# Kernel tuning notes

Measured on AMD Instinct MI355X. Metric: run time of the kernel, lower is better.

The kernel has to match this reference:

```python
import jax, jax.numpy as jnp
import numpy as np

B = 2
SEQ = 384            # args.seq_len (per-stock sub-sequence length)
N_AUX = 4            # len(args.aux_tickers)
S = SEQ * N_AUX + 1  # global separator token + tiled sub-sequences
D_MODEL = 512
NHEAD = 8
HEAD_DIM = 64
ROPE = 32            # qk_rope_dim
KV_C = 256
Q_C = 384
D_FF = 1536
H2 = NHEAD * 2       # differential attention sub-heads
DH = HEAD_DIM // 2
RH = ROPE // 2
EPS = 1.1920929e-07  # torch RMSNorm default eps (fp32 machine eps)
SCALING = 1.0 / ((HEAD_DIM + ROPE) // 2)
LAMBDA_INIT = 0.8 - 0.6 * float(np.exp(-0.3 * 0))  # depth=0 -> 0.2


def rmsnorm(x, w, eps=EPS):
    return x * jax.lax.rsqrt(jnp.mean(jnp.square(x), -1, keepdims=True) + eps) * w


def apply_rope(xs, cos, sin):
    # xs: [B, N_AUX, SEQ, H2, RH]; cos/sin: [SEQ, RH//2]
    xr = xs[..., 0::2]
    xi = xs[..., 1::2]
    c = cos[None, None, :, None, :]
    s = sin[None, None, :, None, :]
    yr = xr * c - xi * s
    yi = xr * s + xi * c
    return jnp.stack([yr, yi], axis=-1).reshape(xs.shape)


def _build_mask():
    causal = np.triu(np.ones((SEQ, SEQ), np.bool_), 1)
    tiled = np.tile(causal, (N_AUX, N_AUX))
    m = np.ones((S, S), np.bool_)
    m[:, 0] = False          # everyone attends to global separator
    m[1:, 1:] = tiled
    return jnp.asarray(m)[None, None]  # [1,1,S,S], True = masked


MASK = _build_mask()


def setup_inputs() -> dict:
    key = jax.random.key(0)
    ks = jax.random.split(key, 16)

    def w(k, shape, std=0.02):
        return jax.random.normal(k, shape, jnp.float32) * std

    x = jax.random.normal(ks[0], (B, S, D_MODEL), jnp.float32)
    # rope table: complex [SEQ, ROPE//4] stored as (cos, sin)
    pairs = ROPE // 4
    inv = 1.0 / (10000.0 ** (np.arange(pairs, dtype=np.float64) / pairs))
    ang = np.outer(np.arange(SEQ), inv)
    freqs = jnp.asarray(np.stack([np.cos(ang), np.sin(ang)], -1), jnp.float32)
    return {
        'x': x,
        'freqs': freqs,
        'W_kv_down': w(ks[1], (D_MODEL, KV_C + ROPE)),
        'W_q_down': w(ks[2], (D_MODEL, Q_C)),
        'W_kv_up': w(ks[3], (KV_C, NHEAD * HEAD_DIM * 2)),
        'W_q_up': w(ks[4], (Q_C, NHEAD * (HEAD_DIM + ROPE))),
        'kv_norm_w': jnp.ones((KV_C,), jnp.float32),
        'q_norm_w': jnp.ones((Q_C,), jnp.float32),
        'W_o': w(ks[5], (NHEAD * HEAD_DIM, D_MODEL)),
        'lambda_q1': w(ks[6], (DH,), 0.1),
        'lambda_k1': w(ks[7], (DH,), 0.1),
        'lambda_q2': w(ks[8], (DH,), 0.1),
        'lambda_k2': w(ks[9], (DH,), 0.1),
        'head_norm_w': jnp.ones((HEAD_DIM,), jnp.float32),
        'norm1_w': jnp.ones((D_MODEL,), jnp.float32),
        'norm2_w': jnp.ones((D_MODEL,), jnp.float32),
        'W_ff_in': w(ks[10], (D_MODEL, 2 * D_FF)),
        'W_ff_out': w(ks[11], (D_FF, D_MODEL)),
    }


def reference(x, freqs, W_kv_down, W_q_down, W_kv_up, W_q_up, kv_norm_w, q_norm_w,
              W_o, lambda_q1, lambda_k1, lambda_q2, lambda_k2, head_norm_w,
              norm1_w, norm2_w, W_ff_in, W_ff_out):
    cos, sin = freqs[..., 0], freqs[..., 1]
    # ---- attention block (pre-norm) ----
    h = rmsnorm(x, norm1_w)
    ckv_full = h @ W_kv_down                               # [B,S,KV_C+ROPE]
    c_kv, k_rope = ckv_full[..., :KV_C], ckv_full[..., KV_C:]
    kv = (rmsnorm(c_kv, kv_norm_w) @ W_kv_up).reshape(B, S, NHEAD, 2 * HEAD_DIM)
    k, v = kv[..., :HEAD_DIM], kv[..., HEAD_DIM:]
    k = k.reshape(B, S, H2, DH)
    qf = (rmsnorm(h @ W_q_down, q_norm_w) @ W_q_up).reshape(B, S, NHEAD, HEAD_DIM + ROPE)
    q, q_rope = qf[..., :HEAD_DIM], qf[..., HEAD_DIM:]
    q = q.reshape(B, S, H2, DH)
    k_rope = jnp.broadcast_to(k_rope[:, :, None, :], (B, S, NHEAD, ROPE)).reshape(B, S, H2, RH)
    q_rope = q_rope.reshape(B, S, H2, RH)
    # split off global separator token, rope per sub-sequence
    q_sep, q_rot = q_rope[:, :1], q_rope[:, 1:].reshape(B, N_AUX, SEQ, H2, RH)
    k_sep, k_rot = k_rope[:, :1], k_rope[:, 1:].reshape(B, N_AUX, SEQ, H2, RH)
    q_rot = apply_rope(q_rot, cos, sin).reshape(B, S - 1, H2, RH)
    k_rot = apply_rope(k_rot, cos, sin).reshape(B, S - 1, H2, RH)
    q_rope = jnp.concatenate([q_sep, q_rot], axis=1)
    k_rope = jnp.concatenate([k_sep, k_rot], axis=1)
    qh = jnp.concatenate([q, q_rope], -1).transpose(0, 2, 1, 3)  # [B,H2,S,DH+RH]
    kh = jnp.concatenate([k, k_rope], -1).transpose(0, 2, 1, 3)
    a = jnp.einsum('bhqd,bhkd->bhqk', qh, kh) * SCALING
    abs_a = jnp.where(MASK, -1e9, jnp.abs(a))
    p = jnp.sign(a) * jax.nn.softmax(abs_a, axis=-1)
    lam = (jnp.exp(jnp.sum(lambda_q1 * lambda_k1)) -
           jnp.exp(jnp.sum(lambda_q2 * lambda_k2)) + LAMBDA_INIT)
    p = p.reshape(B, NHEAD, 2, S, S)
    G = jnp.mean(p[:, :, 0], axis=-1, keepdims=True)
    att = p[:, :, 0] - lam * p[:, :, 1] + G * lam
    att = jnp.where(MASK, 0.0, att)
    o = jnp.einsum('bhqk,bkhd->bqhd', att, v)              # [B,S,NHEAD,HEAD_DIM]
    o = rmsnorm(o, head_norm_w, 1e-5).reshape(B, S, NHEAD * HEAD_DIM)
    x = x + o @ W_o
    # ---- SwiGLU FFN ----
    h2 = rmsnorm(x, norm2_w)
    uv = h2 @ W_ff_in
    u, g = uv[..., :D_FF], uv[..., D_FF:]
    return x + (u * jax.nn.silu(g)) @ W_ff_out
```

## Files before the change

kernel.cpp:

```cpp
#include <hip/hip_runtime.h>

#define NB 2
#define SEQN 384
#define NS 1537
#define NS_PAD 1600
#define NH 8
#define H2N 16
#define NM (NB*NS)
#define DFF 1536
#define EPS1 1.1920929e-07f
#define SCAL (1.0f/48.0f)
#define SC2 (SCAL * 1.4426950408889634f)

typedef __bf16 bf16x8 __attribute__((ext_vector_type(8)));
typedef _Float16 f16x8 __attribute__((ext_vector_type(8)));
typedef float f32x4 __attribute__((ext_vector_type(4)));

__device__ __forceinline__ unsigned short f2bf(float f) {
    unsigned int u = __builtin_bit_cast(unsigned int, f);
    u += 0x7FFFu + ((u >> 16) & 1u);
    return (unsigned short)(u >> 16);
}
__device__ __forceinline__ float bf2f(unsigned short h) {
    unsigned int u = ((unsigned int)h) << 16;
    return __builtin_bit_cast(float, u);
}

struct TD { const float* w; unsigned short* hi; unsigned short* lo; int K; int N; };
struct TD7 { TD d[7]; int tend[7]; };

__global__ __launch_bounds__(256) void transpose_all(TD7 a) {
    __shared__ float tile[32][33];
    int t = blockIdx.x;
    int i = 0;
    while (t >= a.tend[i]) i++;
    int base = (i == 0) ? 0 : a.tend[i - 1];
    int lt = t - base;
    const float* w = a.d[i].w;
    unsigned short* hi = a.d[i].hi;
    unsigned short* lo = a.d[i].lo;
    int K = a.d[i].K, N = a.d[i].N;
    int kt = (K + 31) / 32;
    int k0 = (lt % kt) * 32, n0 = (lt / kt) * 32;
    int tx = threadIdx.x & 31, ty4 = (threadIdx.x >> 5) * 4;
    for (int q = 0; q < 4; q++) {
        int k = k0 + ty4 + q, n = n0 + tx;
        tile[ty4 + q][tx] = (k < K && n < N) ? w[(size_t)k * N + n] : 0.f;
    }
    __syncthreads();
    for (int q = 0; q < 4; q++) {
        int n = n0 + ty4 + q, k = k0 + tx;
        if (n < N && k < K) {
            float v = tile[tx][ty4 + q];
            unsigned short hb = f2bf(v);
            size_t o = (size_t)n * K + k;
            hi[o] = hb;
            if (lo) lo[o] = f2bf(v - bf2f(hb));
        }
    }
}

__global__ void lam_kernel(const float* q1, const float* k1, const float* q2, const float* k2,
                           float* out) {
    int t = threadIdx.x;
    float p1 = 0.f, p2 = 0.f;
    if (t < 32) { p1 = q1[t] * k1[t]; p2 = q2[t] * k2[t]; }
    for (int o = 1; o < 32; o <<= 1) { p1 += __shfl_xor(p1, o); p2 += __shfl_xor(p2, o); }
    if (t == 0) out[0] = expf(p1) - expf(p2) + 0.2f;
}

__global__ __launch_bounds__(256) void rmsnorm_k(const float* __restrict__ in,
    const float* __restrict__ w, unsigned short* __restrict__ hi, unsigned short* __restrict__ lo,
    int in_stride, int C, float eps) {
    int row = blockIdx.x;
    const float* x = in + (size_t)row * in_stride;
    float ss = 0.f;
    for (int j = threadIdx.x; j < C; j += 256) { float v = x[j]; ss += v * v; }
    for (int o = 1; o < 64; o <<= 1) ss += __shfl_xor(ss, o);
    __shared__ float red[4];
    if ((threadIdx.x & 63) == 0) red[threadIdx.x >> 6] = ss;
    __syncthreads();
    ss = red[0] + red[1] + red[2] + red[3];
    float rs = rsqrtf(ss / (float)C + eps);
    for (int j = threadIdx.x; j < C; j += 256) {
        float y = x[j] * rs * w[j];
        unsigned short hb = f2bf(y);
        hi[(size_t)row * C + j] = hb;
        if (lo) lo[(size_t)row * C + j] = f2bf(y - bf2f(hb));
    }
}

__global__ __launch_bounds__(256) void gemm_single(const unsigned short* __restrict__ A,
    const unsigned short* __restrict__ Bt, float* __restrict__ C_, const float* __restrict__ res,
    int M, int N, int K) {
    __shared__ unsigned short As[128][32];
    __shared__ unsigned short Bs[64][32];
    int m0 = blockIdx.x * 128, n0 = blockIdx.y * 64;
    int tid = threadIdx.x;
    int lane = tid & 63, wid = tid >> 6;
    int wr = wid >> 1, wc = wid & 1;
    int r = lane & 15, g = lane >> 4;
    int lrow = tid >> 2, lk = (tid & 3) * 8;
    f32x4 acc[4][2] = {};
    int ar0 = m0 + lrow, ar1 = m0 + 64 + lrow, brow = n0 + lrow;
    bool a0ok = ar0 < M, a1ok = ar1 < M, bok = brow < N;
    size_t a0off = (size_t)ar0 * K + lk, a1off = (size_t)ar1 * K + lk, boff = (size_t)brow * K + lk;
    for (int k0 = 0; k0 < K; k0 += 32) {
        uint4 av0 = {0,0,0,0}, av1 = {0,0,0,0}, bv = {0,0,0,0};
        if (a0ok) av0 = *(const uint4*)(A + a0off + k0);
        if (a1ok) av1 = *(const uint4*)(A + a1off + k0);
        if (bok)  bv  = *(const uint4*)(Bt + boff + k0);
        __syncthreads();
        *(uint4*)&As[lrow][lk] = av0;
        *(uint4*)&As[64 + lrow][lk] = av1;
        *(uint4*)&Bs[lrow][lk] = bv;
        __syncthreads();
        bf16x8 a[4], bb[2];
        #pragma unroll
        for (int i = 0; i < 4; i++) a[i] = *(const bf16x8*)&As[wr * 64 + i * 16 + r][g * 8];
        #pragma unroll
        for (int j = 0; j < 2; j++) bb[j] = *(const bf16x8*)&Bs[wc * 32 + j * 16 + r][g * 8];
        #pragma unroll
        for (int i = 0; i < 4; i++)
            #pragma unroll
            for (int j = 0; j < 2; j++)
                acc[i][j] = __builtin_amdgcn_mfma_f32_16x16x32_bf16(a[i], bb[j], acc[i][j], 0, 0, 0);
    }
    #pragma unroll
    for (int i = 0; i < 4; i++)
        #pragma unroll
        for (int j = 0; j < 2; j++) {
            int col = n0 + wc * 32 + j * 16 + r;
            if (col >= N) continue;
            #pragma unroll
            for (int e = 0; e < 4; e++) {
                int row = m0 + wr * 64 + i * 16 + g * 4 + e;
                if (row >= M) continue;
                float v = acc[i][j][e];
                if (res) v += res[(size_t)row * N + col];
                C_[(size_t)row * N + col] = v;
            }
        }
}

__global__ __launch_bounds__(256) void gemm_x3(const unsigned short* __restrict__ Ah,
    const unsigned short* __restrict__ Al, const unsigned short* __restrict__ Bh,
    const unsigned short* __restrict__ Bl, float* __restrict__ C_, int M, int N, int K) {
    __shared__ unsigned short AsH[128][32], AsL[128][32], BsH[64][32], BsL[64][32];
    int m0 = blockIdx.x * 128, n0 = blockIdx.y * 64;
    int tid = threadIdx.x;
    int lane = tid & 63, wid = tid >> 6;
    int wr = wid >> 1, wc = wid & 1;
    int r = lane & 15, g = lane >> 4;
    int lrow = tid >> 2, lk = (tid & 3) * 8;
    f32x4 acc[4][2] = {};
    int ar0 = m0 + lrow, ar1 = m0 + 64 + lrow, brow = n0 + lrow;
    bool a0ok = ar0 < M, a1ok = ar1 < M, bok = brow < N;
    size_t a0off = (size_t)ar0 * K + lk, a1off = (size_t)ar1 * K + lk, boff = (size_t)brow * K + lk;
    for (int k0 = 0; k0 < K; k0 += 32) {
        uint4 ah0 = {0,0,0,0}, al0 = {0,0,0,0}, ah1 = {0,0,0,0}, al1 = {0,0,0,0};
        uint4 bh0 = {0,0,0,0}, bl0 = {0,0,0,0};
        if (a0ok) { ah0 = *(const uint4*)(Ah + a0off + k0); al0 = *(const uint4*)(Al + a0off + k0); }
        if (a1ok) { ah1 = *(const uint4*)(Ah + a1off + k0); al1 = *(const uint4*)(Al + a1off + k0); }
        if (bok)  { bh0 = *(const uint4*)(Bh + boff + k0);  bl0 = *(const uint4*)(Bl + boff + k0); }
        __syncthreads();
        *(uint4*)&AsH[lrow][lk] = ah0; *(uint4*)&AsH[64 + lrow][lk] = ah1;
        *(uint4*)&AsL[lrow][lk] = al0; *(uint4*)&AsL[64 + lrow][lk] = al1;
        *(uint4*)&BsH[lrow][lk] = bh0; *(uint4*)&BsL[lrow][lk] = bl0;
        __syncthreads();
        bf16x8 ah[4], al[4], bh[2], bl[2];
        #pragma unroll
        for (int i = 0; i < 4; i++) {
            ah[i] = *(const bf16x8*)&AsH[wr * 64 + i * 16 + r][g * 8];
            al[i] = *(const bf16x8*)&AsL[wr * 64 + i * 16 + r][g * 8];
        }
        #pragma unroll
        for (int j = 0; j < 2; j++) {
            bh[j] = *(const bf16x8*)&BsH[wc * 32 + j * 16 + r][g * 8];
            bl[j] = *(const bf16x8*)&BsL[wc * 32 + j * 16 + r][g * 8];
        }
        #pragma unroll
        for (int i = 0; i < 4; i++)
            #pragma unroll
            for (int j = 0; j < 2; j++) {
                acc[i][j] = __builtin_amdgcn_mfma_f32_16x16x32_bf16(al[i], bh[j], acc[i][j], 0, 0, 0);
                acc[i][j] = __builtin_amdgcn_mfma_f32_16x16x32_bf16(ah[i], bl[j], acc[i][j], 0, 0, 0);
                acc[i][j] = __builtin_amdgcn_mfma_f32_16x16x32_bf16(ah[i], bh[j], acc[i][j], 0, 0, 0);
            }
    }
    #pragma unroll
    for (int i = 0; i < 4; i++)
        #pragma unroll
        for (int j = 0; j < 2; j++) {
            int col = n0 + wc * 32 + j * 16 + r;
            if (col >= N) continue;
            #pragma unroll
            for (int e = 0; e < 4; e++) {
                int row = m0 + wr * 64 + i * 16 + g * 4 + e;
                if (row < M) C_[(size_t)row * N + col] = acc[i][j][e];
            }
        }
}

__global__ void assemble2(const float* __restrict__ qf_, const float* __restrict__ kvf,
    const float* __restrict__ ckv, const float* __restrict__ freqs,
    _Float16* __restrict__ qgh, _Float16* __restrict__ qgl,
    _Float16* __restrict__ kgh, _Float16* __restrict__ kgl) {
    size_t idx = (size_t)blockIdx.x * 256 + threadIdx.x;
    const size_t total = (size_t)NB * H2N * NS_PAD * 32;
    if (idx >= total) return;
    int j2 = (int)(idx & 31);
    size_t t = idx >> 5;
    int s = (int)(t % NS_PAD); size_t r = t / NS_PAD;
    int sub = (int)(r & 1); r >>= 1;
    int h = (int)(r & 7); int b = (int)(r >> 3);
    float2 qv = make_float2(0.f, 0.f), kv2 = make_float2(0.f, 0.f);
    if (s < NS && j2 < 24) {
        size_t bs = (size_t)b * NS + s;
        if (j2 < 16) {
            const float* qp = qf_ + bs * 768 + h * 96 + sub * 32 + j2 * 2;
            qv = make_float2(qp[0], qp[1]);
            const float* kp = kvf + bs * 1024 + h * 128 + sub * 32 + j2 * 2;
            kv2 = make_float2(kp[0], kp[1]);
        } else {
            int i = j2 - 16;
            const float* qp = qf_ + bs * 768 + h * 96 + 64 + sub * 16 + 2 * i;
            float xr = qp[0], xi = qp[1];
            const float* kp = ckv + bs * 288 + 256 + sub * 16 + 2 * i;
            float yr = kp[0], yi = kp[1];
            if (s == 0) {
                qv = make_float2(xr, xi);
                kv2 = make_float2(yr, yi);
            } else {
                int pos = (s - 1) % SEQN;
                float c = freqs[pos * 16 + 2 * i], sn = freqs[pos * 16 + 2 * i + 1];
                qv = make_float2(xr * c - xi * sn, xr * sn + xi * c);
                kv2 = make_float2(yr * c - yi * sn, yr * sn + yi * c);
            }
        }
    }
    _Float16 qx = (_Float16)qv.x, qy = (_Float16)qv.y;
    _Float16 kx = (_Float16)kv2.x, ky = (_Float16)kv2.y;
    qgh[idx * 2] = qx; qgh[idx * 2 + 1] = qy;
    kgh[idx * 2] = kx; kgh[idx * 2 + 1] = ky;
    qgl[idx * 2] = (_Float16)(qv.x - (float)qx); qgl[idx * 2 + 1] = (_Float16)(qv.y - (float)qy);
    kgl[idx * 2] = (_Float16)(kv2.x - (float)kx); kgl[idx * 2 + 1] = (_Float16)(kv2.y - (float)ky);
}

__global__ __launch_bounds__(256) void vtrans(const float* __restrict__ kvf,
                                              _Float16* __restrict__ vt) {
    __shared__ float tile[64][65];
    int k0 = blockIdx.x * 64;
    int b = blockIdx.y >> 3, h = blockIdx.y & 7;
    int tid = threadIdx.x;
    int row = tid >> 2, cq = (tid & 3) * 16;
    for (int i = 0; i < 16; i++) {
        int key = k0 + row;
        tile[row][cq + i] = (key < NS)
            ? kvf[((size_t)(b * NS + key)) * 1024 + h * 128 + 64 + cq + i] : 0.f;
    }
    __syncthreads();
    int d = tid >> 2, kq = (tid & 3) * 16;
    for (int i = 0; i < 16; i++)
        vt[((size_t)((b * 8 + h) * 64 + d)) * NS_PAD + k0 + kq + i] = (_Float16)tile[kq + i][d];
}

__global__ __launch_bounds__(256) void prefix2_k(const float* __restrict__ kvf,
                                                 float* __restrict__ P4) {
    __shared__ float tot[4][64];
    int bh = blockIdx.x; int b = bh >> 3, h = bh & 7;
    int d = threadIdx.x & 63, ps = threadIdx.x >> 6;
    int p0 = ps * 96;
    float run = 0.f;
    for (int i = 0; i < 96; i++) {
        int p = p0 + i;
        float s = 0.f;
        #pragma unroll
        for (int c = 0; c < 4; c++)
            s += kvf[((size_t)(b * NS + 1 + c * SEQN + p)) * 1024 + h * 128 + 64 + d];
        run += s;
        P4[((size_t)bh * SEQN + p) * 64 + d] = run;
    }
    tot[ps][d] = run;
    __syncthreads();
    if (ps > 0) {
        float off = 0.f;
        for (int j = 0; j < ps; j++) off += tot[j][d];
        for (int i = 0; i < 96; i++)
            P4[((size_t)bh * SEQN + p0 + i) * 64 + d] += off;
    }
}

__global__ __launch_bounds__(256) void flash_split(
    const _Float16* __restrict__ qgh, const _Float16* __restrict__ qgl,
    const _Float16* __restrict__ kgh, const _Float16* __restrict__ kgl,
    const _Float16* __restrict__ vt,
    float* __restrict__ Opart, float* __restrict__ zpart) {
    __shared__ _Float16 Ksh[2][64][72];
    __shared__ _Float16 Ksl[2][64][72];
    __shared__ _Float16 Vt[64][72];
    __shared__ _Float16 Pl[4][16][72];
    const int tile = blockIdx.x;
    const int h = blockIdx.y & 7, split = blockIdx.y >> 3;
    const int b = blockIdx.z;
    const int bh = b * 8 + h;
    const int qs0 = tile * 64;
    const int tid = threadIdx.x;
    const int wave = tid >> 6, lane = tid & 63;
    const int r = lane & 15, g = lane >> 4;
    const int qrow = qs0 + wave * 16;
    const size_t sh0 = (size_t)(bh * 2);

    f16x8 qfh[2][2], qfl[2][2];
    #pragma unroll
    for (int sub = 0; sub < 2; sub++)
        #pragma unroll
        for (int ks = 0; ks < 2; ks++) {
            size_t off = ((sh0 + sub) * NS_PAD + qrow + r) * 64 + ks * 32 + g * 8;
            qfh[sub][ks] = *(const f16x8*)(qgh + off);
            qfl[sub][ks] = *(const f16x8*)(qgl + off);
        }

    float z0p[4] = {0.f,0.f,0.f,0.f}, g0p[4] = {0.f,0.f,0.f,0.f}, z1p[4] = {0.f,0.f,0.f,0.f};
    f32x4 O0[4], O1[4];
    #pragma unroll
    for (int e = 0; e < 4; e++) { O0[e] = (f32x4){0.f,0.f,0.f,0.f}; O1[e] = (f32x4){0.f,0.f,0.f,0.f}; }
    int qpos[4];
    #pragma unroll
    for (int e = 0; e < 4; e++) {
        int q = qrow + g * 4 + e;
        qpos[e] = (q == 0) ? -1 : (q - 1) % SEQN;
    }
    int lo = qs0 < 1 ? 1 : qs0;
    int hi = qs0 + 63 < NS - 1 ? qs0 + 63 : NS - 1;
    int maxpos = ((lo - 1) / SEQN != (hi - 1) / SEQN) ? (SEQN - 1) : (hi - 1) % SEQN;

    for (int c = 2 * split; c < 2 * split + 2; c++) {
        int nb = (c == 0) ? ((maxpos + 2 + 63) >> 6) : ((maxpos + 1 + 63) >> 6);
        int kstart = (c == 0) ? 0 : (c * SEQN + 1);
        int cbase = c * SEQN + 1;
        for (int j = 0; j < nb; j++) {
            int kbase = kstart + j * 64;
            __syncthreads();
            #pragma unroll
            for (int i = 0; i < 4; i++) {
                int chunk = i * 256 + tid;
                int arr = chunk >> 9;
                int cc = chunk & 511;
                int row = cc >> 3, c8 = (cc & 7) * 8;
                size_t goff = ((sh0 + arr) * NS_PAD + kbase + row) * 64 + c8;
                *(uint4*)&Ksh[arr][row][c8] = *(const uint4*)(kgh + goff);
                *(uint4*)&Ksl[arr][row][c8] = *(const uint4*)(kgl + goff);
            }
            #pragma unroll
            for (int i = 0; i < 2; i++) {
                int cc = i * 256 + tid;
                int d = cc >> 3, c8 = (cc & 7) * 8;
                *(uint4*)&Vt[d][c8] =
                    *(const uint4*)(vt + ((size_t)(bh * 64 + d)) * NS_PAD + kbase + c8);
            }
            __syncthreads();

            f16x8 bv[4][2];
            #pragma unroll
            for (int dt = 0; dt < 4; dt++)
                #pragma unroll
                for (int ks = 0; ks < 2; ks++)
                    bv[dt][ks] = *(const f16x8*)&Vt[dt * 16 + r][ks * 32 + g * 8];

            bool um[4][4];
            #pragma unroll
            for (int t4 = 0; t4 < 4; t4++) {
                int kk2 = kbase + t4 * 16 + r;
                int rel = kk2 - cbase;
                #pragma unroll
                for (int e = 0; e < 4; e++)
                    um[e][t4] = (kk2 == 0) ||
                                ((unsigned)rel < (unsigned)SEQN && rel <= qpos[e]);
            }

            #pragma unroll
            for (int sub = 0; sub < 2; sub++) {
                f32x4 acc[4];
                #pragma unroll
                for (int t4 = 0; t4 < 4; t4++) acc[t4] = (f32x4){0.f,0.f,0.f,0.f};
                #pragma unroll
                for (int t4 = 0; t4 < 4; t4++)
                    #pragma unroll
                    for (int ks = 0; ks < 2; ks++) {
                        f16x8 bkh = *(const f16x8*)&Ksh[sub][t4 * 16 + r][ks * 32 + g * 8];
                        f16x8 bkl = *(const f16x8*)&Ksl[sub][t4 * 16 + r][ks * 32 + g * 8];
                        acc[t4] = __builtin_amdgcn_mfma_f32_16x16x32_f16(qfl[sub][ks], bkh, acc[t4], 0, 0, 0);
                        acc[t4] = __builtin_amdgcn_mfma_f32_16x16x32_f16(qfh[sub][ks], bkl, acc[t4], 0, 0, 0);
                        acc[t4] = __builtin_amdgcn_mfma_f32_16x16x32_f16(qfh[sub][ks], bkh, acc[t4], 0, 0, 0);
                    }
                #pragma unroll
                for (int e = 0; e < 4; e++) {
                    #pragma unroll
                    for (int t4 = 0; t4 < 4; t4++) {
                        float a = acc[t4][e];
                        float ef = exp2f(fabsf(a) * SC2);
                        float ev = um[e][t4] ? ef : 0.f;
                        float pvv = copysignf(ev, a);
                        if (sub == 0) { z0p[e] += ev; g0p[e] += pvv; }
                        else          { z1p[e] += ev; }
                        Pl[wave][g * 4 + e][t4 * 16 + r] = (_Float16)pvv;
                    }
                }
                __builtin_amdgcn_wave_barrier();
                f16x8 pa0 = *(const f16x8*)&Pl[wave][r][g * 8];
                f16x8 pa1 = *(const f16x8*)&Pl[wave][r][32 + g * 8];
                #pragma unroll
                for (int dt = 0; dt < 4; dt++) {
                    if (sub == 0) {
                        O0[dt] = __builtin_amdgcn_mfma_f32_16x16x32_f16(pa0, bv[dt][0], O0[dt], 0, 0, 0);
                        O0[dt] = __builtin_amdgcn_mfma_f32_16x16x32_f16(pa1, bv[dt][1], O0[dt], 0, 0, 0);
                    } else {
                        O1[dt] = __builtin_amdgcn_mfma_f32_16x16x32_f16(pa0, bv[dt][0], O1[dt], 0, 0, 0);
                        O1[dt] = __builtin_amdgcn_mfma_f32_16x16x32_f16(pa1, bv[dt][1], O1[dt], 0, 0, 0);
                    }
                }
            }
        }
    }

    #pragma unroll
    for (int e = 0; e < 4; e++) {
        float z0 = z0p[e], g0 = g0p[e], z1 = z1p[e];
        #pragma unroll
        for (int o = 1; o < 16; o <<= 1) {
            z0 += __shfl_xor(z0, o); g0 += __shfl_xor(g0, o); z1 += __shfl_xor(z1, o);
        }
        int q = qrow + g * 4 + e;
        if (q < NS) {
            if (r == 0) {
                float* zp = zpart + (((size_t)split * 16 + bh) * NS + q) * 4;
                zp[0] = z0; zp[1] = g0; zp[2] = z1;
            }
            float* op = Opart + (((size_t)split * 16 + bh) * NS + q) * 128;
            #pragma unroll
            for (int dt = 0; dt < 4; dt++) {
                op[dt * 16 + r] = O0[dt][e];
                op[64 + dt * 16 + r] = O1[dt][e];
            }
        }
    }
}

__global__ __launch_bounds__(256) void combine_attn(const float* __restrict__ Opart,
    const float* __restrict__ zpart, const float* __restrict__ kvf,
    const float* __restrict__ P4, const float* __restrict__ lamp,
    const float* __restrict__ hw, unsigned short* __restrict__ o_n) {
    int b = blockIdx.z, h = blockIdx.y, bh = b * 8 + h;
    int ql = threadIdx.x >> 2, dp = threadIdx.x & 3;
    int q = blockIdx.x * 64 + ql;
    bool ok = q < NS;
    int qc = ok ? q : 0;
    float lam = lamp[0];
    size_t i0 = ((size_t)0 * 16 + bh) * NS + qc;
    size_t i1 = ((size_t)1 * 16 + bh) * NS + qc;
    const float* za = zpart + i0 * 4;
    const float* zb = zpart + i1 * 4;
    float z0 = za[0] + zb[0], g0 = za[1] + zb[1], z1 = za[2] + zb[2];
    float iz0 = 1.f / z0;
    float l1 = lam / z1;
    float Gl = lam * g0 * iz0 * (1.f / (float)NS);
    int qpos = (q == 0) ? -1 : (q - 1) % SEQN;
    const float* oa = Opart + i0 * 128 + dp * 16;
    const float* ob = Opart + i1 * 128 + dp * 16;
    float of[16]; float ss = 0.f;
    #pragma unroll
    for (int i = 0; i < 16; i++) {
        int d = dp * 16 + i;
        float O0 = oa[i] + ob[i];
        float O1 = oa[64 + i] + ob[64 + i];
        float vs = kvf[((size_t)(b * NS)) * 1024 + h * 128 + 64 + d];
        if (qpos >= 0) vs += P4[((size_t)bh * SEQN + qpos) * 64 + d];
        float o = O0 * iz0 - O1 * l1 + Gl * vs;
        of[i] = o; ss += o * o;
    }
    ss += __shfl_xor(ss, 1); ss += __shfl_xor(ss, 2);
    float rs = rsqrtf(ss / 64.f + 1e-5f);
    if (ok) {
        unsigned int pk[8];
        #pragma unroll
        for (int i = 0; i < 8; i++) {
            unsigned int a = f2bf(of[2 * i] * rs * hw[dp * 16 + 2 * i]);
            unsigned int c = f2bf(of[2 * i + 1] * rs * hw[dp * 16 + 2 * i + 1]);
            pk[i] = a | (c << 16);
        }
        unsigned short* dst = o_n + ((size_t)(b * NS + q)) * 512 + h * 64 + dp * 16;
        *(uint4*)dst = *(uint4*)&pk[0];
        *(uint4*)(dst + 8) = *(uint4*)&pk[4];
    }
}

__global__ void swiglu_k(const float* __restrict__ uv, unsigned short* __restrict__ act) {
    size_t idx = (size_t)blockIdx.x * 256 + threadIdx.x;
    if (idx >= (size_t)NM * DFF) return;
    size_t mrow = idx / DFF; int j = (int)(idx % DFF);
    float u = uv[mrow * (2 * DFF) + j];
    float gg = uv[mrow * (2 * DFF) + DFF + j];
    float sg = gg / (1.f + __expf(-gg));
    act[idx] = f2bf(u * sg);
}

extern "C" void kernel_launch(void* const* d_in, const int* in_sizes, int n_in,
                              void* d_out, int out_size, void* d_ws, size_t ws_size,
                              hipStream_t stream) {
    (void)in_sizes; (void)n_in; (void)out_size; (void)ws_size;
    const float* x    = (const float*)d_in[0];
    const float* freqs= (const float*)d_in[1];
    const float* Wkvd = (const float*)d_in[2];
    const float* Wqd  = (const float*)d_in[3];
    const float* Wkvu = (const float*)d_in[4];
    const float* Wqu  = (const float*)d_in[5];
    const float* kvnw = (const float*)d_in[6];
    const float* qnw  = (const float*)d_in[7];
    const float* Wo   = (const float*)d_in[8];
    const float* lq1  = (const float*)d_in[9];
    const float* lk1  = (const float*)d_in[10];
    const float* lq2  = (const float*)d_in[11];
    const float* lk2  = (const float*)d_in[12];
    const float* hnw  = (const float*)d_in[13];
    const float* n1w  = (const float*)d_in[14];
    const float* n2w  = (const float*)d_in[15];
    const float* Wffi = (const float*)d_in[16];
    const float* Wffo = (const float*)d_in[17];
    float* out = (float*)d_out;

    char* p = (char*)d_ws;
    auto alloc = [&](size_t nbytes) -> char* {
        char* r = p; p += (nbytes + 255) & ~(size_t)255; return r;
    };
    unsigned short* wkvd_h = (unsigned short*)alloc((size_t)512 * 288 * 2);
    unsigned short* wkvd_l = (unsigned short*)alloc((size_t)512 * 288 * 2);
    unsigned short* wqd_h  = (unsigned short*)alloc((size_t)512 * 384 * 2);
    unsigned short* wqd_l  = (unsigned short*)alloc((size_t)512 * 384 * 2);
    unsigned short* wkvu_h = (unsigned short*)alloc((size_t)256 * 1024 * 2);
    unsigned short* wkvu_l = (unsigned short*)alloc((size_t)256 * 1024 * 2);
    unsigned short* wqu_h  = (unsigned short*)alloc((size_t)384 * 768 * 2);
    unsigned short* wqu_l  = (unsigned short*)alloc((size_t)384 * 768 * 2);
    unsigned short* wo_h   = (unsigned short*)alloc((size_t)512 * 512 * 2);
    unsigned short* wffi_h = (unsigned short*)alloc((size_t)512 * 3072 * 2);
    unsigned short* wffo_h = (unsigned short*)alloc((size_t)1536 * 512 * 2);
    unsigned short* h_hi   = (unsigned short*)alloc((size_t)NM * 512 * 2);
    unsigned short* h_lo   = (unsigned short*)alloc((size_t)NM * 512 * 2);
    char* cq0 = p;
    float* ckv = (float*)alloc((size_t)NM * 288 * 4);
    float* qd  = (float*)alloc((size_t)NM * 384 * 4);
    float* x2  = (float*)cq0;
    char* nb0 = p;
    unsigned short* ckvn_h = (unsigned short*)alloc((size_t)NM * 256 * 2);
    unsigned short* ckvn_l = (unsigned short*)alloc((size_t)NM * 256 * 2);
    unsigned short* qdn_h  = (unsigned short*)alloc((size_t)NM * 384 * 2);
    unsigned short* qdn_l  = (unsigned short*)alloc((size_t)NM * 384 * 2);
    unsigned short* o_n    = (unsigned short*)alloc((size_t)NM * 512 * 2);
    unsigned short* h2     = (unsigned short*)alloc((size_t)NM * 512 * 2);
    unsigned short* act    = (unsigned short*)nb0;
    char* r0 = p;
    float* kvf = (float*)alloc((size_t)NM * 1024 * 4);
    float* qff = (float*)alloc((size_t)NM * 768 * 4);
    _Float16* qgh = (_Float16*)alloc((size_t)NB * H2N * NS_PAD * 64 * 2);
    _Float16* qgl = (_Float16*)alloc((size_t)NB * H2N * NS_PAD * 64 * 2);
    _Float16* kgh = (_Float16*)alloc((size_t)NB * H2N * NS_PAD * 64 * 2);
    _Float16* kgl = (_Float16*)alloc((size_t)NB * H2N * NS_PAD * 64 * 2);
    _Float16* vt  = (_Float16*)alloc((size_t)NB * NH * 64 * NS_PAD * 2);
    float* P4     = (float*)alloc((size_t)NB * NH * SEQN * 64 * 4);
    float* Opart  = (float*)alloc((size_t)2 * 16 * NS * 128 * 4);
    float* zpart  = (float*)alloc((size_t)2 * 16 * NS * 4 * 4);
    float* uv     = (float*)r0;
    float* lamv   = (float*)alloc(256);

    {
        TD7 a;
        const float* ws_[7] = {Wkvd, Wqd, Wkvu, Wqu, Wo, Wffi, Wffo};
        unsigned short* his[7] = {wkvd_h, wqd_h, wkvu_h, wqu_h, wo_h, wffi_h, wffo_h};
        unsigned short* los[7] = {wkvd_l, wqd_l, wkvu_l, wqu_l, nullptr, nullptr, nullptr};
        int Ks[7] = {512, 512, 256, 384, 512, 512, 1536};
        int Ns[7] = {288, 384, 1024, 768, 512, 3072, 512};
        int cum = 0;
        for (int i = 0; i < 7; i++) {
            a.d[i] = TD{ws_[i], his[i], los[i], Ks[i], Ns[i]};
            cum += ((Ks[i] + 31) / 32) * ((Ns[i] + 31) / 32);
            a.tend[i] = cum;
        }
        transpose_all<<<dim3(cum), 256, 0, stream>>>(a);
    }
    lam_kernel<<<1, 64, 0, stream>>>(lq1, lk1, lq2, lk2, lamv);

    rmsnorm_k<<<NM, 256, 0, stream>>>(x, n1w, h_hi, h_lo, 512, 512, EPS1);

    const int GX = (NM + 127) / 128;
    gemm_x3<<<dim3(GX, (288 + 63) / 64), 256, 0, stream>>>(h_hi, h_lo, wkvd_h, wkvd_l, ckv, NM, 288, 512);
    gemm_x3<<<dim3(GX, (384 + 63) / 64), 256, 0, stream>>>(h_hi, h_lo, wqd_h, wqd_l, qd, NM, 384, 512);

    rmsnorm_k<<<NM, 256, 0, stream>>>(ckv, kvnw, ckvn_h, ckvn_l, 288, 256, EPS1);
    rmsnorm_k<<<NM, 256, 0, stream>>>(qd, qnw, qdn_h, qdn_l, 384, 384, EPS1);

    gemm_x3<<<dim3(GX, 1024 / 64), 256, 0, stream>>>(ckvn_h, ckvn_l, wkvu_h, wkvu_l, kvf, NM, 1024, 256);
    gemm_x3<<<dim3(GX, 768 / 64), 256, 0, stream>>>(qdn_h, qdn_l, wqu_h, wqu_l, qff, NM, 768, 384);

    {
        size_t total = (size_t)NB * H2N * NS_PAD * 32;
        assemble2<<<dim3((unsigned)((total + 255) / 256)), 256, 0, stream>>>(
            qff, kvf, ckv, freqs, qgh, qgl, kgh, kgl);
    }
    vtrans<<<dim3(NS_PAD / 64, NB * NH), 256, 0, stream>>>(kvf, vt);
    prefix2_k<<<dim3(NB * NH), 256, 0, stream>>>(kvf, P4);

    flash_split<<<dim3((NS + 63) / 64, 16, NB), 256, 0, stream>>>(
        qgh, qgl, kgh, kgl, vt, Opart, zpart);
    combine_attn<<<dim3((NS + 63) / 64, NH, NB), 256, 0, stream>>>(
        Opart, zpart, kvf, P4, lamv, hnw, o_n);

    gemm_single<<<dim3(GX, 512 / 64), 256, 0, stream>>>(o_n, wo_h, x2, x, NM, 512, 512);
    rmsnorm_k<<<NM, 256, 0, stream>>>(x2, n2w, h2, nullptr, 512, 512, EPS1);
    gemm_single<<<dim3(GX, 3072 / 64), 256, 0, stream>>>(h2, wffi_h, uv, nullptr, NM, 3072, 512);
    {
        size_t total = (size_t)NM * DFF;
        swiglu_k<<<dim3((unsigned)((total + 255) / 256)), 256, 0, stream>>>(uv, act);
    }
    gemm_single<<<dim3(GX, 512 / 64), 256, 0, stream>>>(act, wffo_h, out, x2, NM, 512, 1536);
}
```

Measured before the change: 333.2 us.

## Swizzle flash LDS tiles, pad GEMM LDS rows, interleave key blocks across splits

Replaces the padded LDS arrays in the flash attention kernel with an XOR-swizzled 64-column layout for K, V and P tiles, aiming to reduce bank conflicts while saving shared memory. The GEMM LDS tiles get row padding (32 to 40) to break bank conflicts on fragment reads. The two attention splits now take alternating key blocks across all four chunks instead of two chunks each, which balances causal work between the splits. The risk is that the swizzle costs extra index arithmetic, and the interleaved split walks every chunk's loop bounds.

Result: slower. 344.4 us (+3.4%).

```diff
diff --git a/kernel.cpp b/kernel.cpp
--- a/kernel.cpp
+++ b/kernel.cpp
@@ -11,6 +11,8 @@
 #define EPS1 1.1920929e-07f
 #define SCAL (1.0f/48.0f)
 #define SC2 (SCAL * 1.4426950408889634f)
+
+#define SWZ(row, col) ((((row) << 6)) + ((col) ^ (((row) & 7) << 3)))
 
 typedef __bf16 bf16x8 __attribute__((ext_vector_type(8)));
 typedef _Float16 f16x8 __attribute__((ext_vector_type(8)));
@@ -93,8 +95,8 @@
 __global__ __launch_bounds__(256) void gemm_single(const unsigned short* __restrict__ A,
     const unsigned short* __restrict__ Bt, float* __restrict__ C_, const float* __restrict__ res,
     int M, int N, int K) {
-    __shared__ unsigned short As[128][32];
-    __shared__ unsigned short Bs[64][32];
+    __shared__ unsigned short As[128][40];
+    __shared__ unsigned short Bs[64][40];
     int m0 = blockIdx.x * 128, n0 = blockIdx.y * 64;
     int tid = threadIdx.x;
     int lane = tid & 63, wid = tid >> 6;
@@ -146,7 +148,7 @@
 __global__ __launch_bounds__(256) void gemm_x3(const unsigned short* __restrict__ Ah,
     const unsigned short* __restrict__ Al, const unsigned short* __restrict__ Bh,
     const unsigned short* __restrict__ Bl, float* __restrict__ C_, int M, int N, int K) {
-    __shared__ unsigned short AsH[128][32], AsL[128][32], BsH[64][32], BsL[64][32];
+    __shared__ unsigned short AsH[128][40], AsL[128][40], BsH[64][40], BsL[64][40];
     int m0 = blockIdx.x * 128, n0 = blockIdx.y * 64;
     int tid = threadIdx.x;
     int lane = tid & 63, wid = tid >> 6;
@@ -296,10 +298,10 @@
     const _Float16* __restrict__ kgh, const _Float16* __restrict__ kgl,
     const _Float16* __restrict__ vt,
     float* __restrict__ Opart, float* __restrict__ zpart) {
-    __shared__ _Float16 Ksh[2][64][72];
-    __shared__ _Float16 Ksl[2][64][72];
-    __shared__ _Float16 Vt[64][72];
-    __shared__ _Float16 Pl[4][16][72];
+    __shared__ _Float16 Ksh[2][64 * 64];
+    __shared__ _Float16 Ksl[2][64 * 64];
+    __shared__ _Float16 Vt[64 * 64];
+    __shared__ _Float16 Pl[4][16 * 64];
     const int tile = blockIdx.x;
     const int h = blockIdx.y & 7, split = blockIdx.y >> 3;
     const int b = blockIdx.z;
@@ -335,11 +337,13 @@
     int hi = qs0 + 63 < NS - 1 ? qs0 + 63 : NS - 1;
     int maxpos = ((lo - 1) / SEQN != (hi - 1) / SEQN) ? (SEQN - 1) : (hi - 1) % SEQN;
 
-    for (int c = 2 * split; c < 2 * split + 2; c++) {
+    int cnt = 0;
+    for (int c = 0; c < 4; c++) {
         int nb = (c == 0) ? ((maxpos + 2 + 63) >> 6) : ((maxpos + 1 + 63) >> 6);
         int kstart = (c == 0) ? 0 : (c * SEQN + 1);
         int cbase = c * SEQN + 1;
-        for (int j = 0; j < nb; j++) {
+        for (int j = 0; j < nb; j++, cnt++) {
+            if ((cnt & 1) != split) continue;
             int kbase = kstart + j * 64;
             __syncthreads();
             #pragma unroll
@@ -349,14 +353,15 @@
                 int cc = chunk & 511;
                 int row = cc >> 3, c8 = (cc & 7) * 8;
                 size_t goff = ((sh0 + arr) * NS_PAD + kbase + row) * 64 + c8;
-                *(uint4*)&Ksh[arr][row][c8] = *(const uint4*)(kgh + goff);
-                *(uint4*)&Ksl[arr][row][c8] = *(const uint4*)(kgl + goff);
+                int di = SWZ(row, c8);
+                *(uint4*)&Ksh[arr][di] = *(const uint4*)(kgh + goff);
+                *(uint4*)&Ksl[arr][di] = *(const uint4*)(kgl + goff);
             }
             #pragma unroll
             for (int i = 0; i < 2; i++) {
                 int cc = i * 256 + tid;
                 int d = cc >> 3, c8 = (cc & 7) * 8;
-                *(uint4*)&Vt[d][c8] =
+                *(uint4*)&Vt[SWZ(d, c8)] =
                     *(const uint4*)(vt + ((size_t)(bh * 64 + d)) * NS_PAD + kbase + c8);
             }
             __syncthreads();
@@ -366,7 +371,7 @@
             for (int dt = 0; dt < 4; dt++)
                 #pragma unroll
                 for (int ks = 0; ks < 2; ks++)
-                    bv[dt][ks] = *(const f16x8*)&Vt[dt * 16 + r][ks * 32 + g * 8];
+                    bv[dt][ks] = *(const f16x8*)&Vt[SWZ(dt * 16 + r, ks * 32 + g * 8)];
 
             bool um[4][4];
             #pragma unroll
@@ -388,8 +393,9 @@
                 for (int t4 = 0; t4 < 4; t4++)
                     #pragma unroll
                     for (int ks = 0; ks < 2; ks++) {
-                        f16x8 bkh = *(const f16x8*)&Ksh[sub][t4 * 16 + r][ks * 32 + g * 8];
-                        f16x8 bkl = *(const f16x8*)&Ksl[sub][t4 * 16 + r][ks * 32 + g * 8];
+                        int ki = SWZ(t4 * 16 + r, ks * 32 + g * 8);
+                        f16x8 bkh = *(const f16x8*)&Ksh[sub][ki];
+                        f16x8 bkl = *(const f16x8*)&Ksl[sub][ki];
                         acc[t4] = __builtin_amdgcn_mfma_f32_16x16x32_f16(qfl[sub][ks], bkh, acc[t4], 0, 0, 0);
                         acc[t4] = __builtin_amdgcn_mfma_f32_16x16x32_f16(qfh[sub][ks], bkl, acc[t4], 0, 0, 0);
                         acc[t4] = __builtin_amdgcn_mfma_f32_16x16x32_f16(qfh[sub][ks], bkh, acc[t4], 0, 0, 0);
@@ -404,12 +410,12 @@
                         float pvv = copysignf(ev, a);
                         if (sub == 0) { z0p[e] += ev; g0p[e] += pvv; }
                         else          { z1p[e] += ev; }
-                        Pl[wave][g * 4 + e][t4 * 16 + r] = (_Float16)pvv;
+                        Pl[wave][SWZ(g * 4 + e, t4 * 16 + r)] = (_Float16)pvv;
                     }
                 }
                 __builtin_amdgcn_wave_barrier();
-                f16x8 pa0 = *(const f16x8*)&Pl[wave][r][g * 8];
-                f16x8 pa1 = *(const f16x8*)&Pl[wave][r][32 + g * 8];
+                f16x8 pa0 = *(const f16x8*)&Pl[wave][SWZ(r, g * 8)];
+                f16x8 pa1 = *(const f16x8*)&Pl[wave][SWZ(r, 32 + g * 8)];
                 #pragma unroll
                 for (int dt = 0; dt < 4; dt++) {
                     if (sub == 0) {
```
